# Kernel optimization log

Hardware: AMD Instinct MI355X
Metric: run time of the kernel (lower is better)

Reference implementation:

```python
import jax, jax.numpy as jnp
import numpy as np

B_, H_, W_, DM = 32, 64, 64, 256
D_INNER, D_STATE, NHEADS, HEADDIM = 512, 64, 8, 64
D_IN_PROJ = D_INNER + 2 * D_STATE + NHEADS  # 648


def setup_inputs() -> dict:
    key = jax.random.key(0)
    ks = jax.random.split(key, 4)
    x = jax.random.normal(ks[0], (B_, H_, W_, DM), dtype=jnp.float32)
    W_in = jax.random.normal(ks[1], (DM, D_IN_PROJ), dtype=jnp.float32) * 0.05
    dt_bias = jax.random.normal(ks[2], (NHEADS,), dtype=jnp.float32)
    A_log = jax.random.uniform(ks[3], (NHEADS,), dtype=jnp.float32)  # A in [1, e)
    D_param = jnp.ones((NHEADS,), dtype=jnp.float32)
    ln_gamma = jnp.ones((D_INNER,), dtype=jnp.float32)
    ln_beta = jnp.zeros((D_INNER,), dtype=jnp.float32)
    W_out = jax.random.normal(jax.random.fold_in(key, 7), (D_INNER, DM), dtype=jnp.float32) * 0.05
    return {"x": x, "W_in": W_in, "dt_bias": dt_bias, "A_log": A_log,
            "D_param": D_param, "ln_gamma": ln_gamma, "ln_beta": ln_beta, "W_out": W_out}


def reference(x, W_in, dt_bias, A_log, D_param, ln_gamma, ln_beta, W_out):
    B, H, W, Dm = x.shape
    L = H * W
    u = x.reshape(B, L, Dm)
    A = -jnp.exp(A_log)  # (nheads,), negative
    xbcdt = u @ W_in  # (B, L, 648)
    x_ssm = xbcdt[..., :D_INNER]                          # (B, L, d_inner)
    B_ssm = xbcdt[..., D_INNER:D_INNER + D_STATE]         # (B, L, d_state) ~ K
    C_ssm = xbcdt[..., D_INNER + D_STATE:D_INNER + 2 * D_STATE]  # (B, L, d_state) ~ Q
    dt = jax.nn.softplus(xbcdt[..., D_INNER + 2 * D_STATE:] + dt_bias)  # (B, L, nheads)
    V = x_ssm.reshape(B, L, NHEADS, HEADDIM)  # (B, L, h, p)
    # dA gating: dt * A per head (defaults: no exp/softmax/norm variants)
    dA = dt * A  # (B, L, h)
    V_scaled = V * dA[..., None]  # (B, L, h, p)
    # linear-attention dual: KV = K^T @ V_scaled, then Q @ KV
    KV = jnp.einsum('bls,blhp->bhsp', B_ssm, V_scaled)  # (B, h, d_state, p)
    y = jnp.einsum('bls,bhsp->blhp', C_ssm, KV)         # (B, L, h, p)
    # D skip (per-head)
    y = y + V * D_param[None, None, :, None]
    y = y.reshape(B, L, D_INNER)
    # LayerNorm
    mu = jnp.mean(y, axis=-1, keepdims=True)
    var = jnp.var(y, axis=-1, keepdims=True)
    y = (y - mu) / jnp.sqrt(var + 1e-5) * ln_gamma + ln_beta
    out = y @ W_out
    return out.reshape(B, H, W, Dm)
```

## Files before the change

kernel.cpp:

```cpp
#include <hip/hip_runtime.h>
#include <hip/hip_bf16.h>
#include <math.h>

constexpr int B_N   = 32;
constexpr int L_N   = 4096;
constexpr int DM    = 256;
constexpr int DIN   = 512;
constexpr int DS    = 64;
constexpr int NH    = 8;
constexpr int HD    = 64;
constexpr int M_N   = B_N * L_N;
constexpr int XBW   = 640;
constexpr int YST   = 536;

typedef unsigned short u16;
typedef short s16x4 __attribute__((ext_vector_type(4)));
typedef short s16x8 __attribute__((ext_vector_type(8)));
typedef float f32x4 __attribute__((ext_vector_type(4)));
typedef unsigned short u16x8 __attribute__((ext_vector_type(8)));
typedef unsigned short u16x4 __attribute__((ext_vector_type(4)));

__device__ __forceinline__ float softplusf(float z) {
  return (z > 20.f) ? z : log1pf(expf(z));
}
__device__ __forceinline__ u16 f2bf(float f) {
  unsigned u = __float_as_uint(f);
  u += 0x7FFFu + ((u >> 16) & 1u);
  return (u16)(u >> 16);
}
__device__ __forceinline__ float bf2f(u16 u) {
  return __uint_as_float(((unsigned)u) << 16);
}
__device__ __forceinline__ s16x8 ld_frag2(const short* p) {
  s16x4 lo = *(const s16x4*)p;
  s16x4 hi = *(const s16x4*)(p + 4);
  s16x8 r;
  r[0]=lo[0]; r[1]=lo[1]; r[2]=lo[2]; r[3]=lo[3];
  r[4]=hi[0]; r[5]=hi[1]; r[6]=hi[2]; r[7]=hi[3];
  return r;
}

#define GLDS(gsrc, ldst)                                                       \
  __builtin_amdgcn_global_load_lds(                                            \
      (const __attribute__((address_space(1))) void*)(gsrc),                   \
      (__attribute__((address_space(3))) void*)(ldst), 16, 0, 0)

constexpr long CW1 = 768L * 256;
constexpr long CW2 = CW1 + 256L * 512;
__global__ __launch_bounds__(256) void k_cvt(
    const float* __restrict__ Wi, const float* __restrict__ Wo,
    u16* __restrict__ WinT, u16* __restrict__ WoT) {
  for (long i = (long)blockIdx.x * 256 + threadIdx.x; i < CW2;
       i += (long)gridDim.x * 256) {
    if (i < CW1) {
      int n = (int)(i >> 8); int k = (int)(i & 255);
      WinT[i] = (n < 648) ? f2bf(Wi[(size_t)k * 648 + n]) : (u16)0;
    } else {
      long t = i - CW1; int n = (int)(t >> 9); int k = (int)(t & 511);
      WoT[t] = f2bf(Wo[(size_t)k * 256 + n]);
    }
  }
}

__global__ __launch_bounds__(256) void k_inproj(
    const float* __restrict__ x, const u16* __restrict__ WinT,
    const float* __restrict__ dt_bias, const float* __restrict__ A_log,
    u16* __restrict__ xbcdt, float* __restrict__ dAv) {
  __shared__ __align__(16) short sA[128 * 36];
  __shared__ __align__(16) short sB[128 * 32];
  const int tid = threadIdx.x;
  const int wave = tid >> 6, lane = tid & 63;
  const int m0 = blockIdx.y * 128, n0 = blockIdx.x * 128;
  const int wr = wave >> 1, wc = wave & 1;
  const int fr = lane & 15, fq = lane >> 4;
  f32x4 acc[4][4] = {};

  int rowA[2], kcA[2];
  const u16* gB[2]; int ldsOffB[2];
#pragma unroll
  for (int q = 0; q < 2; ++q) {
    int G = wave * 128 + q * 64 + lane;
    rowA[q] = G >> 2; kcA[q] = G & 3;
    gB[q] = WinT + (size_t)(n0 + (G >> 2)) * DM + (G & 3) * 8;
    ldsOffB[q] = G * 8;
  }

  for (int k0 = 0; k0 < DM; k0 += 32) {
    float4 av[2][2];
#pragma unroll
    for (int q = 0; q < 2; ++q) {
      const float* src = x + (size_t)(m0 + rowA[q]) * DM + k0 + kcA[q] * 8;
      av[q][0] = *(const float4*)src;
      av[q][1] = *(const float4*)(src + 4);
    }
    if (k0) __syncthreads();
#pragma unroll
    for (int q = 0; q < 2; ++q) GLDS(gB[q] + k0, sB + ldsOffB[q]);
#pragma unroll
    for (int q = 0; q < 2; ++q) {
      u16x4 lo = {f2bf(av[q][0].x), f2bf(av[q][0].y), f2bf(av[q][0].z), f2bf(av[q][0].w)};
      u16x4 hi = {f2bf(av[q][1].x), f2bf(av[q][1].y), f2bf(av[q][1].z), f2bf(av[q][1].w)};
      *(u16x4*)&sA[rowA[q] * 36 + kcA[q] * 8]     = lo;
      *(u16x4*)&sA[rowA[q] * 36 + kcA[q] * 8 + 4] = hi;
    }
    __syncthreads();
    const int kb = fq * 8;
    s16x8 af[4], bf[4];
#pragma unroll
    for (int i = 0; i < 4; ++i)
      af[i] = ld_frag2(&sA[(wr * 64 + i * 16 + fr) * 36 + kb]);
#pragma unroll
    for (int j = 0; j < 4; ++j)
      bf[j] = *(const s16x8*)&sB[(wc * 64 + j * 16 + fr) * 32 + kb];
#pragma unroll
    for (int i = 0; i < 4; ++i)
#pragma unroll
      for (int j = 0; j < 4; ++j)
        acc[i][j] = __builtin_amdgcn_mfma_f32_16x16x32_bf16(af[i], bf[j], acc[i][j], 0, 0, 0);
  }

  const int cl = fr;
  const int row_base = m0 + wr * 64 + fq * 4;
  if (n0 < 640) {
    const int col_base = n0 + wc * 64;
#pragma unroll
    for (int i = 0; i < 4; ++i)
#pragma unroll
      for (int r = 0; r < 4; ++r) {
        int row = row_base + i * 16 + r;
#pragma unroll
        for (int j = 0; j < 4; ++j)
          xbcdt[(size_t)row * XBW + col_base + j * 16 + cl] = f2bf(acc[i][j][r]);
      }
  } else if (wc == 0 && cl < 8) {
    const float nAe = -expf(A_log[cl]);
    const float db = dt_bias[cl];
#pragma unroll
    for (int i = 0; i < 4; ++i)
#pragma unroll
      for (int r = 0; r < 4; ++r) {
        int row = row_base + i * 16 + r;
        dAv[(size_t)row * NH + cl] = softplusf(acc[i][0][r] + db) * nAe;
      }
  }
}

__global__ __launch_bounds__(256) void k_bt(
    const u16* __restrict__ xbcdt, u16* __restrict__ Bt) {
  __shared__ u16 sT[64][72];
  const int m0 = blockIdx.x * 64;
  const int b  = m0 >> 12;
  const int l0 = m0 & (L_N - 1);
  const int tid = threadIdx.x;
#pragma unroll
  for (int q = 0; q < 2; ++q) {
    int r = (tid >> 3) + q * 32, c8 = (tid & 7) * 8;
    u16x8 v = *(const u16x8*)&xbcdt[(size_t)(m0 + r) * XBW + DIN + c8];
#pragma unroll
    for (int jj = 0; jj < 8; ++jj) sT[r][c8 + jj] = v[jj];
  }
  __syncthreads();
#pragma unroll
  for (int q = 0; q < 2; ++q) {
    int s = (tid >> 3) + q * 32, lc8 = (tid & 7) * 8;
    u16x8 o;
#pragma unroll
    for (int jj = 0; jj < 8; ++jj) o[jj] = sT[lc8 + jj][s];
    *(u16x8*)&Bt[((size_t)(b * 64 + s)) * L_N + l0 + lc8] = o;
  }
}

__global__ __launch_bounds__(256) void k_kv(
    const u16* __restrict__ xbcdt, const u16* __restrict__ Bt,
    const float* __restrict__ dAv, float* __restrict__ KVp) {
  const int bh = blockIdx.y;
  const int b = bh >> 3, h = bh & 7;
  const int l0 = blockIdx.x * (L_N / 4);
  const int tid = threadIdx.x;
  const int wave = tid >> 6, lane = tid & 63;
  const int wr = wave >> 1, wc = wave & 1;
  const int fr = lane & 15, fq = lane >> 4;
  __shared__ short sBt[64 * 36];
  __shared__ short sVt[64 * 36];
  f32x4 acc[2][2] = {};
  const int ts = tid >> 2, tlc = tid & 3;
  const int tl = tid >> 3, tpg = tid & 7;

  for (int ks = 0; ks < L_N / 4; ks += 32) {
    u16x8 vb = *(const u16x8*)&Bt[((size_t)(b * 64 + ts)) * L_N + l0 + ks + tlc * 8];
    const int gl = b * L_N + l0 + ks + tl;
    u16x8 vv = *(const u16x8*)&xbcdt[(size_t)gl * XBW + h * HD + tpg * 8];
    const float da = dAv[(size_t)gl * NH + h];
    __syncthreads();
    *(s16x4*)&sBt[ts * 36 + tlc * 8]     = *(s16x4*)&vb;
    *(s16x4*)&sBt[ts * 36 + tlc * 8 + 4] = *((s16x4*)&vb + 1);
#pragma unroll
    for (int jj = 0; jj < 8; ++jj)
      sVt[(tpg * 8 + jj) * 36 + tl] = (short)f2bf(bf2f(vv[jj]) * da);
    __syncthreads();
    s16x8 af[2], bf[2];
#pragma unroll
    for (int i = 0; i < 2; ++i)
      af[i] = ld_frag2(&sBt[(wr * 32 + i * 16 + fr) * 36 + fq * 8]);
#pragma unroll
    for (int j = 0; j < 2; ++j)
      bf[j] = ld_frag2(&sVt[(wc * 32 + j * 16 + fr) * 36 + fq * 8]);
#pragma unroll
    for (int i = 0; i < 2; ++i)
#pragma unroll
      for (int j = 0; j < 2; ++j)
        acc[i][j] = __builtin_amdgcn_mfma_f32_16x16x32_bf16(af[i], bf[j], acc[i][j], 0, 0, 0);
  }
  float* dst = KVp + ((size_t)(blockIdx.x * 256 + bh)) * 4096;
#pragma unroll
  for (int i = 0; i < 2; ++i)
#pragma unroll
    for (int j = 0; j < 2; ++j) {
      int p = wc * 32 + j * 16 + fr;
      int s0 = wr * 32 + i * 16 + fq * 4;
      float4 v;
      v.x = acc[i][j][0]; v.y = acc[i][j][1];
      v.z = acc[i][j][2]; v.w = acc[i][j][3];
      *(float4*)&dst[p * 64 + s0] = v;
    }
}

__global__ __launch_bounds__(256) void k_kvsum(
    const float* __restrict__ KVp, u16* __restrict__ KVt) {
  const int bh = blockIdx.x;
  const int tid = threadIdx.x;
  const float* src = KVp + (size_t)bh * 4096;
#pragma unroll
  for (int q = 0; q < 4; ++q) {
    int i4 = (tid + q * 256) * 4;
    float4 v0 = *(const float4*)(src + i4);
    float4 v1 = *(const float4*)(src + 1048576 + i4);
    float4 v2 = *(const float4*)(src + 2097152 + i4);
    float4 v3 = *(const float4*)(src + 3145728 + i4);
    u16x4 o = {f2bf(v0.x + v1.x + v2.x + v3.x),
               f2bf(v0.y + v1.y + v2.y + v3.y),
               f2bf(v0.z + v1.z + v2.z + v3.z),
               f2bf(v0.w + v1.w + v2.w + v3.w)};
    *(u16x4*)&KVt[(size_t)bh * 4096 + i4] = o;
  }
}

__global__ __launch_bounds__(256) void k_fused(
    const u16* __restrict__ xb, const u16* __restrict__ KVt,
    const float* __restrict__ Dp, const float* __restrict__ g,
    const float* __restrict__ bt, const u16* __restrict__ WoT,
    float* __restrict__ out) {
  __shared__ __align__(16) short sC[64 * 76];
  __shared__ __align__(16) short sY[64 * YST];
  const int tid = threadIdx.x;
  const int wave = tid >> 6, lane = tid & 63;
  const int fr = lane & 15, fq = lane >> 4;
  const int m0 = blockIdx.x * 64;
  const int b = m0 >> 12;

#pragma unroll
  for (int q = 0; q < 2; ++q) {
    int idx = tid + q * 256;
    int row = idx >> 3, c8 = (idx & 7) * 8;
    u16x8 v = *(const u16x8*)&xb[(size_t)(m0 + row) * XBW + DIN + DS + c8];
    *(u16x8*)&sC[row * 76 + c8] = v;
  }
  __syncthreads();

#pragma unroll
  for (int hh = 0; hh < 2; ++hh) {
    const int h = wave + hh * 4;
    const u16* kt = KVt + (size_t)(b * NH + h) * 4096;
    f32x4 acc[4][4] = {};
#pragma unroll
    for (int kk = 0; kk < 2; ++kk) {
      s16x8 af[4], bf[4];
#pragma unroll
      for (int i = 0; i < 4; ++i)
        af[i] = *(const s16x8*)&sC[(i * 16 + fr) * 76 + kk * 32 + fq * 8];
#pragma unroll
      for (int j = 0; j < 4; ++j)
        bf[j] = *(const s16x8*)&kt[(j * 16 + fr) * 64 + kk * 32 + fq * 8];
#pragma unroll
      for (int i = 0; i < 4; ++i)
#pragma unroll
        for (int j = 0; j < 4; ++j)
          acc[i][j] = __builtin_amdgcn_mfma_f32_16x16x32_bf16(af[i], bf[j], acc[i][j], 0, 0, 0);
    }
#pragma unroll
    for (int i = 0; i < 4; ++i)
#pragma unroll
      for (int r = 0; r < 4; ++r) {
        int rl = i * 16 + fq * 4 + r;
#pragma unroll
        for (int j = 0; j < 4; ++j)
          sY[rl * YST + h * HD + j * 16 + fr] = (short)f2bf(acc[i][j][r]);
      }
  }
  __syncthreads();

  {
    const int row = tid >> 2, seg4 = tid & 3;
    const u16* vrow = xb + (size_t)(m0 + row) * XBW;
    float s = 0.f, q = 0.f;
#pragma unroll
    for (int c = 0; c < 16; ++c) {
      int k0 = seg4 * 8 + c * 32;
      const float ds = Dp[c >> 1];
      u16x8 v = *(const u16x8*)&sY[row * YST + k0];
      u16x8 w = *(const u16x8*)(vrow + k0);
      u16x8 o;
#pragma unroll
      for (int jj = 0; jj < 8; ++jj) {
        float f = bf2f(v[jj]) + ds * bf2f(w[jj]);
        s += f; q += f * f;
        o[jj] = f2bf(f);
      }
      *(u16x8*)&sY[row * YST + k0] = o;
    }
    s += __shfl_xor(s, 1); q += __shfl_xor(q, 1);
    s += __shfl_xor(s, 2); q += __shfl_xor(q, 2);
    const float mu = s / DIN;
    const float rstd = rsqrtf(q / DIN - mu * mu + 1e-5f);
#pragma unroll
    for (int c = 0; c < 16; ++c) {
      int k0 = seg4 * 8 + c * 32;
      u16x8 v = *(const u16x8*)&sY[row * YST + k0];
      float4 g0 = *(const float4*)(g + k0);
      float4 g1 = *(const float4*)(g + k0 + 4);
      float4 b0 = *(const float4*)(bt + k0);
      float4 b1 = *(const float4*)(bt + k0 + 4);
      u16x8 o;
      o[0] = f2bf((bf2f(v[0]) - mu) * rstd * g0.x + b0.x);
      o[1] = f2bf((bf2f(v[1]) - mu) * rstd * g0.y + b0.y);
      o[2] = f2bf((bf2f(v[2]) - mu) * rstd * g0.z + b0.z);
      o[3] = f2bf((bf2f(v[3]) - mu) * rstd * g0.w + b0.w);
      o[4] = f2bf((bf2f(v[4]) - mu) * rstd * g1.x + b1.x);
      o[5] = f2bf((bf2f(v[5]) - mu) * rstd * g1.y + b1.y);
      o[6] = f2bf((bf2f(v[6]) - mu) * rstd * g1.z + b1.z);
      o[7] = f2bf((bf2f(v[7]) - mu) * rstd * g1.w + b1.w);
      *(u16x8*)&sY[row * YST + k0] = o;
    }
  }
  __syncthreads();

  {
    f32x4 acc2[4][4] = {};
#pragma unroll
    for (int kk = 0; kk < 16; ++kk) {
      s16x8 af2[4], bf2[4];
#pragma unroll
      for (int i = 0; i < 4; ++i)
        af2[i] = *(const s16x8*)&sY[(i * 16 + fr) * YST + kk * 32 + fq * 8];
#pragma unroll
      for (int j = 0; j < 4; ++j)
        bf2[j] = *(const s16x8*)&WoT[(size_t)(wave * 64 + j * 16 + fr) * DIN + kk * 32 + fq * 8];
#pragma unroll
      for (int i = 0; i < 4; ++i)
#pragma unroll
        for (int j = 0; j < 4; ++j)
          acc2[i][j] = __builtin_amdgcn_mfma_f32_16x16x32_bf16(af2[i], bf2[j], acc2[i][j], 0, 0, 0);
    }
#pragma unroll
    for (int i = 0; i < 4; ++i)
#pragma unroll
      for (int r = 0; r < 4; ++r) {
        int row = m0 + i * 16 + fq * 4 + r;
#pragma unroll
        for (int j = 0; j < 4; ++j)
          out[(size_t)row * DM + wave * 64 + j * 16 + fr] = acc2[i][j][r];
      }
  }
}

extern "C" void kernel_launch(void* const* d_in, const int* in_sizes, int n_in,
                              void* d_out, int out_size, void* d_ws, size_t ws_size,
                              hipStream_t stream) {
  const float* x       = (const float*)d_in[0];
  const float* W_in    = (const float*)d_in[1];
  const float* dt_bias = (const float*)d_in[2];
  const float* A_log   = (const float*)d_in[3];
  const float* D_param = (const float*)d_in[4];
  const float* gamma   = (const float*)d_in[5];
  const float* beta    = (const float*)d_in[6];
  const float* W_out   = (const float*)d_in[7];
  float* out = (float*)d_out;

  u16* ws    = (u16*)d_ws;
  u16* WinT  = ws;
  u16* WoT   = WinT + 768L * 256;
  u16* xbcdt = WoT + 256L * 512;
  u16* Bt    = xbcdt + (size_t)M_N * XBW;
  float* dAv = (float*)(Bt + (size_t)B_N * 64 * L_N);
  float* KVp = dAv + (size_t)M_N * NH;
  u16* KVt   = (u16*)(KVp + 4L * 256 * 4096);

  k_cvt    <<<256, 256, 0, stream>>>(W_in, W_out, WinT, WoT);
  k_inproj <<<dim3(6, M_N / 128), 256, 0, stream>>>(x, WinT, dt_bias, A_log, xbcdt, dAv);
  k_bt     <<<M_N / 64, 256, 0, stream>>>(xbcdt, Bt);
  k_kv     <<<dim3(4, B_N * NH), 256, 0, stream>>>(xbcdt, Bt, dAv, KVp);
  k_kvsum  <<<B_N * NH, 256, 0, stream>>>(KVp, KVt);
  k_fused  <<<M_N / 64, 256, 0, stream>>>(xbcdt, KVt, D_param, gamma, beta, WoT, out);
}
```

Measured before the change: 335.6 us.

## Stage full x row tile in LDS once and loop over all N tiles

Measured after the change: 285.1 us. 1.18x faster.

```diff
diff --git a/kernel.cpp b/kernel.cpp
--- a/kernel.cpp
+++ b/kernel.cpp
@@ -12,6 +12,7 @@
 constexpr int M_N   = B_N * L_N;
 constexpr int XBW   = 640;
 constexpr int YST   = 536;
+constexpr int AST   = 268;
 
 typedef unsigned short u16;
 typedef short s16x4 __attribute__((ext_vector_type(4)));
@@ -66,82 +67,78 @@
     const float* __restrict__ x, const u16* __restrict__ WinT,
     const float* __restrict__ dt_bias, const float* __restrict__ A_log,
     u16* __restrict__ xbcdt, float* __restrict__ dAv) {
-  __shared__ __align__(16) short sA[128 * 36];
+  __shared__ __align__(16) short sA[128 * AST];
   __shared__ __align__(16) short sB[128 * 32];
   const int tid = threadIdx.x;
   const int wave = tid >> 6, lane = tid & 63;
-  const int m0 = blockIdx.y * 128, n0 = blockIdx.x * 128;
+  const int m0 = blockIdx.x * 128;
   const int wr = wave >> 1, wc = wave & 1;
   const int fr = lane & 15, fq = lane >> 4;
-  f32x4 acc[4][4] = {};
-
-  int rowA[2], kcA[2];
-  const u16* gB[2]; int ldsOffB[2];
+
+#pragma unroll
+  for (int q = 0; q < 32; ++q) {
+    int idx = tid + q * 256;
+    int row = idx >> 6, c4 = idx & 63;
+    float4 v = *(const float4*)(x + (size_t)(m0 + row) * DM + c4 * 4);
+    u16x4 o = {f2bf(v.x), f2bf(v.y), f2bf(v.z), f2bf(v.w)};
+    *(u16x4*)&sA[row * AST + c4 * 4] = o;
+  }
+  __syncthreads();
+
+  int rowB[2], kcB[2], ldsOffB[2];
 #pragma unroll
   for (int q = 0; q < 2; ++q) {
     int G = wave * 128 + q * 64 + lane;
-    rowA[q] = G >> 2; kcA[q] = G & 3;
-    gB[q] = WinT + (size_t)(n0 + (G >> 2)) * DM + (G & 3) * 8;
+    rowB[q] = G >> 2; kcB[q] = G & 3;
     ldsOffB[q] = G * 8;
   }
 
-  for (int k0 = 0; k0 < DM; k0 += 32) {
-    float4 av[2][2];
-#pragma unroll
-    for (int q = 0; q < 2; ++q) {
-      const float* src = x + (size_t)(m0 + rowA[q]) * DM + k0 + kcA[q] * 8;
-      av[q][0] = *(const float4*)src;
-      av[q][1] = *(const float4*)(src + 4);
-    }
-    if (k0) __syncthreads();
-#pragma unroll
-    for (int q = 0; q < 2; ++q) GLDS(gB[q] + k0, sB + ldsOffB[q]);
-#pragma unroll
-    for (int q = 0; q < 2; ++q) {
-      u16x4 lo = {f2bf(av[q][0].x), f2bf(av[q][0].y), f2bf(av[q][0].z), f2bf(av[q][0].w)};
-      u16x4 hi = {f2bf(av[q][1].x), f2bf(av[q][1].y), f2bf(av[q][1].z), f2bf(av[q][1].w)};
-      *(u16x4*)&sA[rowA[q] * 36 + kcA[q] * 8]     = lo;
-      *(u16x4*)&sA[rowA[q] * 36 + kcA[q] * 8 + 4] = hi;
-    }
-    __syncthreads();
-    const int kb = fq * 8;
-    s16x8 af[4], bf[4];
-#pragma unroll
-    for (int i = 0; i < 4; ++i)
-      af[i] = ld_frag2(&sA[(wr * 64 + i * 16 + fr) * 36 + kb]);
-#pragma unroll
-    for (int j = 0; j < 4; ++j)
-      bf[j] = *(const s16x8*)&sB[(wc * 64 + j * 16 + fr) * 32 + kb];
-#pragma unroll
-    for (int i = 0; i < 4; ++i)
+  for (int nt = 0; nt < 6; ++nt) {
+    const int n0 = nt * 128;
+    f32x4 acc[4][4] = {};
+    for (int k0 = 0; k0 < DM; k0 += 32) {
+      if (nt || k0) __syncthreads();
+#pragma unroll
+      for (int q = 0; q < 2; ++q)
+        GLDS(WinT + (size_t)(n0 + rowB[q]) * DM + kcB[q] * 8 + k0, sB + ldsOffB[q]);
+      __syncthreads();
+      const int kb = fq * 8;
+      s16x8 af[4], bf[4];
+#pragma unroll
+      for (int i = 0; i < 4; ++i)
+        af[i] = ld_frag2(&sA[(wr * 64 + i * 16 + fr) * AST + k0 + kb]);
 #pragma unroll
       for (int j = 0; j < 4; ++j)
-        acc[i][j] = __builtin_amdgcn_mfma_f32_16x16x32_bf16(af[i], bf[j], acc[i][j], 0, 0, 0);
-  }
-
-  const int cl = fr;
-  const int row_base = m0 + wr * 64 + fq * 4;
-  if (n0 < 640) {
-    const int col_base = n0 + wc * 64;
-#pragma unroll
-    for (int i = 0; i < 4; ++i)
-#pragma unroll
-      for (int r = 0; r < 4; ++r) {
-        int row = row_base + i * 16 + r;
+        bf[j] = *(const s16x8*)&sB[(wc * 64 + j * 16 + fr) * 32 + kb];
+#pragma unroll
+      for (int i = 0; i < 4; ++i)
 #pragma unroll
         for (int j = 0; j < 4; ++j)
-          xbcdt[(size_t)row * XBW + col_base + j * 16 + cl] = f2bf(acc[i][j][r]);
-      }
-  } else if (wc == 0 && cl < 8) {
-    const float nAe = -expf(A_log[cl]);
-    const float db = dt_bias[cl];
-#pragma unroll
-    for (int i = 0; i < 4; ++i)
-#pragma unroll
-      for (int r = 0; r < 4; ++r) {
-        int row = row_base + i * 16 + r;
-        dAv[(size_t)row * NH + cl] = softplusf(acc[i][0][r] + db) * nAe;
-      }
+          acc[i][j] = __builtin_amdgcn_mfma_f32_16x16x32_bf16(af[i], bf[j], acc[i][j], 0, 0, 0);
+    }
+    const int row_base = m0 + wr * 64 + fq * 4;
+    if (n0 < 640) {
+      const int col_base = n0 + wc * 64;
+#pragma unroll
+      for (int i = 0; i < 4; ++i)
+#pragma unroll
+        for (int r = 0; r < 4; ++r) {
+          int row = row_base + i * 16 + r;
+#pragma unroll
+          for (int j = 0; j < 4; ++j)
+            xbcdt[(size_t)row * XBW + col_base + j * 16 + fr] = f2bf(acc[i][j][r]);
+        }
+    } else if (wc == 0 && fr < 8) {
+      const float nAe = -expf(A_log[fr]);
+      const float db = dt_bias[fr];
+#pragma unroll
+      for (int i = 0; i < 4; ++i)
+#pragma unroll
+        for (int r = 0; r < 4; ++r) {
+          int row = row_base + i * 16 + r;
+          dAv[(size_t)row * NH + fr] = softplusf(acc[i][0][r] + db) * nAe;
+        }
+    }
   }
 }
 
@@ -396,7 +393,7 @@
   u16* KVt   = (u16*)(KVp + 4L * 256 * 4096);
 
   k_cvt    <<<256, 256, 0, stream>>>(W_in, W_out, WinT, WoT);
-  k_inproj <<<dim3(6, M_N / 128), 256, 0, stream>>>(x, WinT, dt_bias, A_log, xbcdt, dAv);
+  k_inproj <<<M_N / 128, 256, 0, stream>>>(x, WinT, dt_bias, A_log, xbcdt, dAv);
   k_bt     <<<M_N / 64, 256, 0, stream>>>(xbcdt, Bt);
   k_kv     <<<dim3(4, B_N * NH), 256, 0, stream>>>(xbcdt, Bt, dAv, KVp);
   k_kvsum  <<<B_N * NH, 256, 0, stream>>>(KVp, KVt);
```
